# Kernel optimization log

Hardware: AMD Instinct MI355X
Metric: run time of the kernel (lower is better)

The kernel has to match this reference:

```python
import jax, jax.numpy as jnp
import numpy as np

D = 128      # d_hidden
TR = 128     # d_tracker
B = 64       # batch
L = 96       # buffer length (L-1 tokens are shifted; buf[0] is a sentinel)
T = 2 * (L - 1) - 1  # 189 transitions: 95 shifts, 94 reduces


def setup_inputs() -> dict:
    key = jax.random.key(0)
    ks = jax.random.split(key, 9)
    s = 0.1
    buffers = jax.random.normal(ks[0], (L, B, 2 * D), dtype=jnp.float32)
    # valid shift-reduce sequence: S S (R S)^93 R  -> 95 shifts, 94 reduces
    pat = [3, 3] + [2, 3] * (L - 3) + [2]
    assert len(pat) == T
    transitions = jnp.asarray(np.tile(np.array(pat, dtype=np.int32)[:, None], (1, B)))
    # Tracker LSTMCell params (torch gate order i, f, g, o)
    W_ih = jax.random.normal(ks[1], (4 * TR, 3 * D), dtype=jnp.float32) * s
    W_hh = jax.random.normal(ks[2], (4 * TR, TR), dtype=jnp.float32) * s
    b_ih = jax.random.normal(ks[3], (4 * TR,), dtype=jnp.float32) * s
    b_hh = jax.random.normal(ks[4], (4 * TR,), dtype=jnp.float32) * s
    # Composition params (gate order g, i, f1, f2, o)
    Wl = jax.random.normal(ks[5], (5 * D, D), dtype=jnp.float32) * s
    bl = jax.random.normal(ks[6], (5 * D,), dtype=jnp.float32) * s
    Wr = jax.random.normal(ks[7], (5 * D, D), dtype=jnp.float32) * s
    Wt = jax.random.normal(ks[8], (5 * D, TR), dtype=jnp.float32) * s
    return {"buffers": buffers, "transitions": transitions,
            "W_ih": W_ih, "W_hh": W_hh, "b_ih": b_ih, "b_hh": b_hh,
            "Wl": Wl, "bl": bl, "Wr": Wr, "Wt": Wt}


def spinn_forward(buffers, transitions, W_ih, W_hh, b_ih, b_hh, Wl, bl, Wr, Wt):
    Lb, Bb, two_d = buffers.shape
    d = two_d // 2
    tr = W_hh.shape[1]
    bidx = jnp.arange(Bb)

    # fixed-size stack per example; slots 0,1 hold buf[0] padding as in torch
    stack0 = jnp.zeros((Bb, Lb + 2, two_d), dtype=buffers.dtype)
    stack0 = stack0.at[:, 0, :].set(buffers[0]).at[:, 1, :].set(buffers[0])
    sp0 = jnp.full((Bb,), 2, dtype=jnp.int32)        # stack pointer (next free slot)
    bp0 = jnp.full((Bb,), Lb, dtype=jnp.int32)       # buffer size (pop from end)
    th0 = jnp.zeros((Bb, tr), dtype=buffers.dtype)
    tc0 = jnp.zeros((Bb, tr), dtype=buffers.dtype)

    def step(carry, trans):
        stack, sp, bp, th, tc = carry
        buf_top = buffers[bp - 1, bidx]              # [B, 2d] buf[-1]
        s1 = stack[bidx, sp - 1]                     # stack[-1]
        s2 = stack[bidx, sp - 2]                     # stack[-2]
        # tracker LSTMCell on h-parts
        x = jnp.concatenate([buf_top[:, :d], s1[:, :d], s2[:, :d]], axis=1)
        gates = x @ W_ih.T + th @ W_hh.T + (b_ih + b_hh)
        ii, ff, gg, oo = jnp.split(gates, 4, axis=1)
        tc2 = jax.nn.sigmoid(ff) * tc + jax.nn.sigmoid(ii) * jnp.tanh(gg)
        th2 = jax.nn.sigmoid(oo) * jnp.tanh(tc2)
        shift = trans == 3
        red = trans == 2
        # composition (computed for all rows, applied only where red)
        lstm_in = s2[:, :d] @ Wl.T + bl + s1[:, :d] @ Wr.T + th2 @ Wt.T
        g_, i_, f1, f2, o_ = jnp.split(lstm_in, 5, axis=1)
        c = (jax.nn.sigmoid(f1) * s2[:, d:] + jax.nn.sigmoid(f2) * s1[:, d:]
             + jax.nn.sigmoid(i_) * jnp.tanh(g_))
        h = jax.nn.sigmoid(o_) * jnp.tanh(c)
        red_val = jnp.concatenate([h, c], axis=1)
        widx = jnp.where(shift, sp, sp - 2)
        val = jnp.where(shift[:, None], buf_top, red_val)
        mask = shift | red
        cur = stack[bidx, widx]
        stack = stack.at[bidx, widx].set(jnp.where(mask[:, None], val, cur))
        sp = sp + jnp.where(shift, 1, 0).astype(sp.dtype) - jnp.where(red, 1, 0).astype(sp.dtype)
        bp = bp - shift.astype(bp.dtype)
        return (stack, sp, bp, th2, tc2), None

    (stack, sp, bp, th, tc), _ = jax.lax.scan(step, (stack0, sp0, bp0, th0, tc0), transitions)
    return stack[bidx, sp - 1][:, :d]                # h of popped top, [B, d]


def reference(buffers, transitions, W_ih, W_hh, b_ih, b_hh, Wl, bl, Wr, Wt):
    return spinn_forward(buffers, transitions, W_ih, W_hh, b_ih, b_hh, Wl, bl, Wr, Wt)
```

## Files before the change

### kernel.cpp

```cpp
#include <hip/hip_runtime.h>

#define D 128
#define TRK 128
#define NB 64
#define LBUF 96
#define T_STEPS 189
#define NWG 32
#define NTHR 256
#define SLOTS 98

typedef __bf16 bf16x8 __attribute__((ext_vector_type(8)));
typedef float f32x4 __attribute__((ext_vector_type(4)));

__device__ __forceinline__ unsigned short f2bf(float f){
  unsigned x = __builtin_bit_cast(unsigned, f);
  unsigned r = (x + 0x7fffu + ((x >> 16) & 1u)) >> 16;
  return (unsigned short)r;
}
__device__ __forceinline__ float bf2f(unsigned short u){
  unsigned x = ((unsigned)u) << 16;
  return __builtin_bit_cast(float, x);
}
__device__ __forceinline__ float sigf(float x){ return 1.f / (1.f + __expf(-x)); }
__device__ __forceinline__ float tanhfast(float x){ return 1.f - 2.f / (__expf(2.f * x) + 1.f); }

#define WS_BUFH   0u
#define WS_STACKH 1572864u
#define WS_STACKC 3178496u
#define WS_TH     6389760u
#define WS_BAR    6422528u

__device__ __forceinline__ void gbar(unsigned* cnt, unsigned target){
  __syncthreads();
  if (threadIdx.x == 0){
    __hip_atomic_fetch_add(cnt, 1u, __ATOMIC_RELEASE, __HIP_MEMORY_SCOPE_AGENT);
    while (__hip_atomic_load(cnt, __ATOMIC_ACQUIRE, __HIP_MEMORY_SCOPE_AGENT) < target)
      __builtin_amdgcn_s_sleep(1);
  }
  __syncthreads();
}

__global__ __launch_bounds__(NTHR, 1) void spinn_kernel(
    const float* __restrict__ buffers, const int* __restrict__ trans,
    const float* __restrict__ W_ih, const float* __restrict__ W_hh,
    const float* __restrict__ b_ih, const float* __restrict__ b_hh,
    const float* __restrict__ Wl, const float* __restrict__ bl,
    const float* __restrict__ Wr, const float* __restrict__ Wt,
    float* __restrict__ out, unsigned char* __restrict__ ws)
{
  unsigned short* bufh   = (unsigned short*)(ws + WS_BUFH);
  unsigned short* stackh = (unsigned short*)(ws + WS_STACKH);
  float*          stackc = (float*)(ws + WS_STACKC);
  unsigned short* thbuf  = (unsigned short*)(ws + WS_TH);
  unsigned*       barcnt = (unsigned*)(ws + WS_BAR);

  __shared__ alignas(16) unsigned short WA_lds[4 * 4 * 64 * 8];
  __shared__ alignas(16) unsigned short WB_lds[6 * 4 * 64 * 8];
  __shared__ float stage[4][16][32];
  __shared__ float tc_lds[256];
  __shared__ float biasA[16];
  __shared__ float biasB[20];
  __shared__ int tr_lds[64];
  __shared__ int sp_lds[64];
  __shared__ int bp_lds[64];

  const int tid  = threadIdx.x;
  const int blk  = blockIdx.x;
  const int lane = tid & 63;
  const int w    = tid >> 6;
  const int gid  = blk * NTHR + tid;

  for (int idx = tid; idx < 4 * 4 * 64 * 8; idx += NTHR){
    int j = idx & 7, ln = (idx >> 3) & 63, kb = (idx >> 9) & 3, src = idx >> 11;
    int v = ln & 15;
    int col = (v >> 2) * 128 + 4 * blk + (v & 3);
    int k = kb * 32 + (ln >> 4) * 8 + j;
    float val = (src < 3) ? W_ih[col * 384 + src * 128 + k] : W_hh[col * 128 + k];
    WA_lds[idx] = f2bf(val);
  }
  for (int idx = tid; idx < 6 * 4 * 64 * 8; idx += NTHR){
    int j = idx & 7, ln = (idx >> 3) & 63, kb = (idx >> 9) & 3, Tt = (idx >> 11) & 1, src = idx >> 12;
    int v = ln & 15;
    int k = kb * 32 + (ln >> 4) * 8 + j;
    float val = 0.f;
    if (Tt == 0){
      int col = (v >> 2) * 128 + 4 * blk + (v & 3);
      const float* Wm = (src == 0) ? Wl : ((src == 1) ? Wr : Wt);
      val = Wm[col * 128 + k];
    } else if ((v >> 2) == 0){
      int col = 512 + 4 * blk + (v & 3);
      const float* Wm = (src == 0) ? Wl : ((src == 1) ? Wr : Wt);
      val = Wm[col * 128 + k];
    }
    WB_lds[idx] = f2bf(val);
  }
  if (tid < 16){ int col = (tid >> 2) * 128 + 4 * blk + (tid & 3); biasA[tid] = b_ih[col] + b_hh[col]; }
  if (tid < 20){
    int col = (tid < 16) ? ((tid >> 2) * 128 + 4 * blk + (tid & 3)) : (512 + 4 * blk + (tid - 16));
    biasB[tid] = bl[col];
  }
  tc_lds[tid] = 0.f;
  if (tid < 64){ sp_lds[tid] = 2; bp_lds[tid] = LBUF; }

  for (int i = gid; i < LBUF * NB * D; i += NWG * NTHR){
    int k = i & 127; int rb = i >> 7;
    bufh[i] = f2bf(buffers[rb * 256 + k]);
  }
  for (int i = gid; i < NB * D; i += NWG * NTHR){
    int b = i >> 7, k = i & 127;
    unsigned short h = f2bf(buffers[b * 256 + k]);
    float c = buffers[b * 256 + 128 + k];
    stackh[(b * SLOTS + 0) * 128 + k] = h;
    stackh[(b * SLOTS + 1) * 128 + k] = h;
    stackc[(b * SLOTS + 0) * 128 + k] = c;
    stackc[(b * SLOTS + 1) * 128 + k] = c;
  }
  for (int i = gid; i < 2 * NB * TRK; i += NWG * NTHR) thbuf[i] = 0;

  unsigned barn = 0;
  gbar(barcnt, ++barn * NWG);

  const bf16x8* WAf = (const bf16x8*)WA_lds;
  const bf16x8* WBf = (const bf16x8*)WB_lds;
  const int r    = w * 16 + (lane & 15);
  const int koff = (lane >> 4) * 8;
  const int dl   = lane >> 4;
  const int dim  = 4 * blk + dl;

  for (int t = 0; t < T_STEPS; ++t){
    if (tid < 64) tr_lds[tid] = trans[t * 64 + tid];
    __syncthreads();
    const int anyRed = __syncthreads_or((tid < 64) && (tr_lds[tid] == 2));
    const unsigned short* th_rd = thbuf + (t & 1) * NB * TRK;
    unsigned short*       th_wr = thbuf + ((t + 1) & 1) * NB * TRK;

    {
      int sp_r = sp_lds[r], bp_r = bp_lds[r];
      const unsigned short* pb = bufh   + ((bp_r - 1) * 64 + r) * 128 + koff;
      const unsigned short* p1 = stackh + (r * SLOTS + sp_r - 1) * 128 + koff;
      const unsigned short* p2 = stackh + (r * SLOTS + sp_r - 2) * 128 + koff;
      const unsigned short* pt = th_rd  + r * 128 + koff;
      bf16x8 a0[4], a1[4], a2[4], a3[4];
      #pragma unroll
      for (int kb = 0; kb < 4; kb++){
        a0[kb] = *(const bf16x8*)(pb + kb * 32);
        a1[kb] = *(const bf16x8*)(p1 + kb * 32);
        a2[kb] = *(const bf16x8*)(p2 + kb * 32);
        a3[kb] = *(const bf16x8*)(pt + kb * 32);
      }
      f32x4 acc = {0.f, 0.f, 0.f, 0.f};
      #pragma unroll
      for (int kb = 0; kb < 4; kb++) acc = __builtin_amdgcn_mfma_f32_16x16x32_bf16(a0[kb], WAf[(0 * 4 + kb) * 64 + lane], acc, 0, 0, 0);
      #pragma unroll
      for (int kb = 0; kb < 4; kb++) acc = __builtin_amdgcn_mfma_f32_16x16x32_bf16(a1[kb], WAf[(1 * 4 + kb) * 64 + lane], acc, 0, 0, 0);
      #pragma unroll
      for (int kb = 0; kb < 4; kb++) acc = __builtin_amdgcn_mfma_f32_16x16x32_bf16(a2[kb], WAf[(2 * 4 + kb) * 64 + lane], acc, 0, 0, 0);
      #pragma unroll
      for (int kb = 0; kb < 4; kb++) acc = __builtin_amdgcn_mfma_f32_16x16x32_bf16(a3[kb], WAf[(3 * 4 + kb) * 64 + lane], acc, 0, 0, 0);
      #pragma unroll
      for (int j = 0; j < 4; j++) stage[w][(lane >> 4) * 4 + j][lane & 15] = acc[j];
    }
    __syncthreads();
    {
      int r16 = lane & 15;
      float iv = stage[w][r16][0 + dl]  + biasA[0 + dl];
      float fv = stage[w][r16][4 + dl]  + biasA[4 + dl];
      float gv = stage[w][r16][8 + dl]  + biasA[8 + dl];
      float ov = stage[w][r16][12 + dl] + biasA[12 + dl];
      float tco = tc_lds[r * 4 + dl];
      float tc2 = sigf(fv) * tco + sigf(iv) * tanhfast(gv);
      float th2 = sigf(ov) * tanhfast(tc2);
      tc_lds[r * 4 + dl] = tc2;
      th_wr[r * 128 + dim] = f2bf(th2);
      if (tr_lds[r] == 3){
        int slot = sp_lds[r]; int bp_r = bp_lds[r];
        stackh[(r * SLOTS + slot) * 128 + dim] = bufh[((bp_r - 1) * 64 + r) * 128 + dim];
        stackc[(r * SLOTS + slot) * 128 + dim] = buffers[((bp_r - 1) * 64 + r) * 256 + 128 + dim];
      }
    }
    gbar(barcnt, ++barn * NWG);

    if (anyRed){
      {
        int sp_r = sp_lds[r];
        const unsigned short* p2 = stackh + (r * SLOTS + sp_r - 2) * 128 + koff;
        const unsigned short* p1 = stackh + (r * SLOTS + sp_r - 1) * 128 + koff;
        const unsigned short* pt = th_wr + r * 128 + koff;
        bf16x8 a0[4], a1[4], a2[4];
        #pragma unroll
        for (int kb = 0; kb < 4; kb++){
          a0[kb] = *(const bf16x8*)(p2 + kb * 32);
          a1[kb] = *(const bf16x8*)(p1 + kb * 32);
          a2[kb] = *(const bf16x8*)(pt + kb * 32);
        }
        f32x4 acc0 = {0.f, 0.f, 0.f, 0.f}, acc1 = {0.f, 0.f, 0.f, 0.f};
        #pragma unroll
        for (int kb = 0; kb < 4; kb++){
          acc0 = __builtin_amdgcn_mfma_f32_16x16x32_bf16(a0[kb], WBf[(0 * 4 + kb) * 64 + lane], acc0, 0, 0, 0);
          acc1 = __builtin_amdgcn_mfma_f32_16x16x32_bf16(a0[kb], WBf[(1 * 4 + kb) * 64 + lane], acc1, 0, 0, 0);
          acc0 = __builtin_amdgcn_mfma_f32_16x16x32_bf16(a1[kb], WBf[(2 * 4 + kb) * 64 + lane], acc0, 0, 0, 0);
          acc1 = __builtin_amdgcn_mfma_f32_16x16x32_bf16(a1[kb], WBf[(3 * 4 + kb) * 64 + lane], acc1, 0, 0, 0);
          acc0 = __builtin_amdgcn_mfma_f32_16x16x32_bf16(a2[kb], WBf[(4 * 4 + kb) * 64 + lane], acc0, 0, 0, 0);
          acc1 = __builtin_amdgcn_mfma_f32_16x16x32_bf16(a2[kb], WBf[(5 * 4 + kb) * 64 + lane], acc1, 0, 0, 0);
        }
        #pragma unroll
        for (int j = 0; j < 4; j++){
          stage[w][(lane >> 4) * 4 + j][lane & 15]      = acc0[j];
          stage[w][(lane >> 4) * 4 + j][16 + (lane & 15)] = acc1[j];
        }
      }
      __syncthreads();
      {
        int r16 = lane & 15;
        int sp_r = sp_lds[r];
        float gv  = stage[w][r16][0 + dl]  + biasB[0 + dl];
        float iv  = stage[w][r16][4 + dl]  + biasB[4 + dl];
        float f1v = stage[w][r16][8 + dl]  + biasB[8 + dl];
        float f2v = stage[w][r16][12 + dl] + biasB[12 + dl];
        float ov  = stage[w][r16][16 + dl] + biasB[16 + dl];
        float s2c = stackc[(r * SLOTS + sp_r - 2) * 128 + dim];
        float s1c = stackc[(r * SLOTS + sp_r - 1) * 128 + dim];
        float c = sigf(f1v) * s2c + sigf(f2v) * s1c + sigf(iv) * tanhfast(gv);
        float h = sigf(ov) * tanhfast(c);
        if (tr_lds[r] == 2){
          stackh[(r * SLOTS + sp_r - 2) * 128 + dim] = f2bf(h);
          stackc[(r * SLOTS + sp_r - 2) * 128 + dim] = c;
        }
      }
      gbar(barcnt, ++barn * NWG);
    }

    if (tid < 64){
      int tr = tr_lds[tid];
      sp_lds[tid] += (tr == 3) - (tr == 2);
      bp_lds[tid] -= (tr == 3);
    }
    __syncthreads();
  }

  {
    int rr = tid & 63, dle = tid >> 6;
    int dme = 4 * blk + dle;
    out[rr * 128 + dme] = bf2f(stackh[(rr * SLOTS + sp_lds[rr] - 1) * 128 + dme]);
  }
}

extern "C" void kernel_launch(void* const* d_in, const int* in_sizes, int n_in,
                              void* d_out, int out_size, void* d_ws, size_t ws_size,
                              hipStream_t stream){
  const float* buffers = (const float*)d_in[0];
  const int*   trans   = (const int*)d_in[1];
  const float* W_ih    = (const float*)d_in[2];
  const float* W_hh    = (const float*)d_in[3];
  const float* b_ih    = (const float*)d_in[4];
  const float* b_hh    = (const float*)d_in[5];
  const float* Wl      = (const float*)d_in[6];
  const float* bl      = (const float*)d_in[7];
  const float* Wr      = (const float*)d_in[8];
  const float* Wt      = (const float*)d_in[9];
  unsigned char* ws = (unsigned char*)d_ws;
  hipMemsetAsync(ws + WS_BAR, 0, 128, stream);
  spinn_kernel<<<dim3(NWG), dim3(NTHR), 0, stream>>>(
      buffers, trans, W_ih, W_hh, b_ih, b_hh, Wl, bl, Wr, Wt,
      (float*)d_out, ws);
}
```

Baseline: 1.661 ms.

## Partition batch into independent groups with per-group flag barriers and register weights

Restructures the persistent kernel from 32 workgroups of 256 threads into 64 single-wave workgroups arranged as 8 batch groups of 8 rows. Each group of 8 workgroups synchronises only among itself through per-workgroup epoch flags, replacing the grid-wide atomic counter barrier. The composition weights move into registers, shared-memory staging of gate values is removed, and cross-workgroup data is exchanged with L2-coherent loads and stores. The aim is to cut global barrier latency and LDS round trips in the serial 189-step loop, at the cost of heavy register pressure and relaxed-ordering synchronisation that could be fragile.

```diff
diff --git a/kernel.cpp b/kernel.cpp
--- a/kernel.cpp
+++ b/kernel.cpp
@@ -5,12 +5,16 @@
 #define NB 64
 #define LBUF 96
 #define T_STEPS 189
-#define NWG 32
-#define NTHR 256
+#define NWG 64
+#define WPG 8
+#define RPG 8
 #define SLOTS 98
 
 typedef __bf16 bf16x8 __attribute__((ext_vector_type(8)));
 typedef float f32x4 __attribute__((ext_vector_type(4)));
+typedef unsigned u32x4 __attribute__((ext_vector_type(4)));
+typedef unsigned short u16x8 __attribute__((ext_vector_type(8)));
+typedef unsigned short u16x4 __attribute__((ext_vector_type(4)));
 
 __device__ __forceinline__ unsigned short f2bf(float f){
   unsigned x = __builtin_bit_cast(unsigned, f);
@@ -24,23 +28,59 @@
 __device__ __forceinline__ float sigf(float x){ return 1.f / (1.f + __expf(-x)); }
 __device__ __forceinline__ float tanhfast(float x){ return 1.f - 2.f / (__expf(2.f * x) + 1.f); }
 
+__device__ __forceinline__ unsigned ld_l3_u32(const unsigned* p){
+  return __hip_atomic_load(p, __ATOMIC_RELAXED, __HIP_MEMORY_SCOPE_AGENT);
+}
+__device__ __forceinline__ bf16x8 ld_l3_frag(const unsigned short* p){
+  const unsigned* q = (const unsigned*)p;
+  u32x4 w;
+  w[0] = ld_l3_u32(q + 0); w[1] = ld_l3_u32(q + 1);
+  w[2] = ld_l3_u32(q + 2); w[3] = ld_l3_u32(q + 3);
+  return __builtin_bit_cast(bf16x8, w);
+}
+__device__ __forceinline__ void st_l3_b16(unsigned short* p, unsigned short v){
+  unsigned vv = v;
+  asm volatile("global_store_short %0, %1, off sc0 sc1" :: "v"(p), "v"(vv) : "memory");
+}
+
 #define WS_BUFH   0u
 #define WS_STACKH 1572864u
 #define WS_STACKC 3178496u
 #define WS_TH     6389760u
-#define WS_BAR    6422528u
-
-__device__ __forceinline__ void gbar(unsigned* cnt, unsigned target){
-  __syncthreads();
-  if (threadIdx.x == 0){
-    __hip_atomic_fetch_add(cnt, 1u, __ATOMIC_RELEASE, __HIP_MEMORY_SCOPE_AGENT);
-    while (__hip_atomic_load(cnt, __ATOMIC_ACQUIRE, __HIP_MEMORY_SCOPE_AGENT) < target)
-      __builtin_amdgcn_s_sleep(1);
-  }
-  __syncthreads();
-}
-
-__global__ __launch_bounds__(NTHR, 1) void spinn_kernel(
+#define WS_FLAGS  6422528u
+#define WS_FLAGS2 6426624u
+
+__device__ __forceinline__ void gbar(unsigned* fl, int sbase, int m, unsigned ep){
+  asm volatile("s_waitcnt vmcnt(0)" ::: "memory");
+  const int l = threadIdx.x;
+  if (l == 0)
+    __hip_atomic_store(fl + (sbase + m) * 16, ep, __ATOMIC_RELAXED, __HIP_MEMORY_SCOPE_AGENT);
+  for (;;){
+    unsigned v = (l < WPG)
+      ? __hip_atomic_load(fl + (sbase + l) * 16, __ATOMIC_RELAXED, __HIP_MEMORY_SCOPE_AGENT)
+      : ep;
+    if (__all((int)(v >= ep))) break;
+    __builtin_amdgcn_s_sleep(1);
+  }
+  __builtin_amdgcn_sched_barrier(0);
+}
+
+__device__ __forceinline__ void gbar_full(unsigned* fl2){
+  asm volatile("s_waitcnt vmcnt(0)" ::: "memory");
+  __builtin_amdgcn_fence(__ATOMIC_RELEASE, "agent");
+  if (threadIdx.x == 0)
+    __hip_atomic_store(fl2 + blockIdx.x * 16, 1u, __ATOMIC_RELAXED, __HIP_MEMORY_SCOPE_AGENT);
+  const int l = threadIdx.x;
+  for (;;){
+    unsigned v = __hip_atomic_load(fl2 + l * 16, __ATOMIC_RELAXED, __HIP_MEMORY_SCOPE_AGENT);
+    if (__all((int)(v >= 1u))) break;
+    __builtin_amdgcn_s_sleep(1);
+  }
+  __builtin_amdgcn_fence(__ATOMIC_ACQUIRE, "agent");
+  __builtin_amdgcn_sched_barrier(0);
+}
+
+__global__ __launch_bounds__(64, 1) void spinn_kernel(
     const float* __restrict__ buffers, const int* __restrict__ trans,
     const float* __restrict__ W_ih, const float* __restrict__ W_hh,
     const float* __restrict__ b_ih, const float* __restrict__ b_hh,
@@ -48,200 +88,204 @@
     const float* __restrict__ Wr, const float* __restrict__ Wt,
     float* __restrict__ out, unsigned char* __restrict__ ws)
 {
-  unsigned short* bufh   = (unsigned short*)(ws + WS_BUFH);
-  unsigned short* stackh = (unsigned short*)(ws + WS_STACKH);
-  float*          stackc = (float*)(ws + WS_STACKC);
-  unsigned short* thbuf  = (unsigned short*)(ws + WS_TH);
-  unsigned*       barcnt = (unsigned*)(ws + WS_BAR);
-
-  __shared__ alignas(16) unsigned short WA_lds[4 * 4 * 64 * 8];
-  __shared__ alignas(16) unsigned short WB_lds[6 * 4 * 64 * 8];
-  __shared__ float stage[4][16][32];
-  __shared__ float tc_lds[256];
-  __shared__ float biasA[16];
-  __shared__ float biasB[20];
-  __shared__ int tr_lds[64];
-  __shared__ int sp_lds[64];
-  __shared__ int bp_lds[64];
-
-  const int tid  = threadIdx.x;
-  const int blk  = blockIdx.x;
-  const int lane = tid & 63;
-  const int w    = tid >> 6;
-  const int gid  = blk * NTHR + tid;
-
-  for (int idx = tid; idx < 4 * 4 * 64 * 8; idx += NTHR){
-    int j = idx & 7, ln = (idx >> 3) & 63, kb = (idx >> 9) & 3, src = idx >> 11;
-    int v = ln & 15;
-    int col = (v >> 2) * 128 + 4 * blk + (v & 3);
-    int k = kb * 32 + (ln >> 4) * 8 + j;
-    float val = (src < 3) ? W_ih[col * 384 + src * 128 + k] : W_hh[col * 128 + k];
-    WA_lds[idx] = f2bf(val);
-  }
-  for (int idx = tid; idx < 6 * 4 * 64 * 8; idx += NTHR){
-    int j = idx & 7, ln = (idx >> 3) & 63, kb = (idx >> 9) & 3, Tt = (idx >> 11) & 1, src = idx >> 12;
-    int v = ln & 15;
-    int k = kb * 32 + (ln >> 4) * 8 + j;
-    float val = 0.f;
-    if (Tt == 0){
-      int col = (v >> 2) * 128 + 4 * blk + (v & 3);
-      const float* Wm = (src == 0) ? Wl : ((src == 1) ? Wr : Wt);
-      val = Wm[col * 128 + k];
-    } else if ((v >> 2) == 0){
-      int col = 512 + 4 * blk + (v & 3);
-      const float* Wm = (src == 0) ? Wl : ((src == 1) ? Wr : Wt);
-      val = Wm[col * 128 + k];
-    }
-    WB_lds[idx] = f2bf(val);
-  }
-  if (tid < 16){ int col = (tid >> 2) * 128 + 4 * blk + (tid & 3); biasA[tid] = b_ih[col] + b_hh[col]; }
-  if (tid < 20){
-    int col = (tid < 16) ? ((tid >> 2) * 128 + 4 * blk + (tid & 3)) : (512 + 4 * blk + (tid - 16));
-    biasB[tid] = bl[col];
-  }
-  tc_lds[tid] = 0.f;
-  if (tid < 64){ sp_lds[tid] = 2; bp_lds[tid] = LBUF; }
-
-  for (int i = gid; i < LBUF * NB * D; i += NWG * NTHR){
-    int k = i & 127; int rb = i >> 7;
-    bufh[i] = f2bf(buffers[rb * 256 + k]);
-  }
-  for (int i = gid; i < NB * D; i += NWG * NTHR){
-    int b = i >> 7, k = i & 127;
-    unsigned short h = f2bf(buffers[b * 256 + k]);
-    float c = buffers[b * 256 + 128 + k];
-    stackh[(b * SLOTS + 0) * 128 + k] = h;
-    stackh[(b * SLOTS + 1) * 128 + k] = h;
-    stackc[(b * SLOTS + 0) * 128 + k] = c;
-    stackc[(b * SLOTS + 1) * 128 + k] = c;
-  }
-  for (int i = gid; i < 2 * NB * TRK; i += NWG * NTHR) thbuf[i] = 0;
-
-  unsigned barn = 0;
-  gbar(barcnt, ++barn * NWG);
-
-  const bf16x8* WAf = (const bf16x8*)WA_lds;
-  const bf16x8* WBf = (const bf16x8*)WB_lds;
-  const int r    = w * 16 + (lane & 15);
-  const int koff = (lane >> 4) * 8;
-  const int dl   = lane >> 4;
-  const int dim  = 4 * blk + dl;
+  const int l = threadIdx.x;
+  const int g = blockIdx.x & 7;
+  const int m = blockIdx.x >> 3;
+  const int tb = g * RPG;
+
+  unsigned short* bufh_g   = (unsigned short*)(ws + WS_BUFH)   + g * (LBUF * RPG * 128);
+  unsigned short* stackh_g = (unsigned short*)(ws + WS_STACKH) + g * (RPG * SLOTS * 128);
+  float*          stackc_w = (float*)(ws + WS_STACKC)          + (g * 8 + m) * (RPG * SLOTS * 16);
+  unsigned short* th_g     = (unsigned short*)(ws + WS_TH)     + g * (2 * RPG * 128);
+  unsigned*       flags    = (unsigned*)(ws + WS_FLAGS);
+  unsigned*       flags2   = (unsigned*)(ws + WS_FLAGS2);
+
+  __shared__ unsigned short WA_lds[32768];
+
+  const int dd = l & 15;
+  const int rf = l & 7;
+  const int k0 = (l >> 4) * 8;
+
+  for (int c0 = l; c0 < 4096; c0 += 64){
+    int ln = c0 & 63, kb = (c0 >> 6) & 3, s = (c0 >> 8) & 3, q = c0 >> 10;
+    int gr = q * 128 + 16 * m + (ln & 15);
+    int kk = kb * 32 + (ln >> 4) * 8;
+    const float* sp = (s < 3) ? (W_ih + gr * 384 + s * 128 + kk) : (W_hh + gr * 128 + kk);
+    f32x4 f0 = *(const f32x4*)sp, f1 = *(const f32x4*)(sp + 4);
+    u16x8 u;
+    #pragma unroll
+    for (int j = 0; j < 4; ++j){ u[j] = f2bf(f0[j]); u[4 + j] = f2bf(f1[j]); }
+    *(u16x8*)(WA_lds + c0 * 8) = u;
+  }
+
+  bf16x8 wb[5][3][4];
+  #pragma unroll
+  for (int p = 0; p < 5; ++p){
+    int gr = (p < 4 ? p * 128 : 512) + 16 * m + dd;
+    #pragma unroll
+    for (int s = 0; s < 3; ++s){
+      const float* base = (s == 0 ? Wl : (s == 1 ? Wr : Wt)) + gr * 128 + k0;
+      #pragma unroll
+      for (int kb = 0; kb < 4; ++kb){
+        f32x4 f0 = *(const f32x4*)(base + kb * 32);
+        f32x4 f1 = *(const f32x4*)(base + kb * 32 + 4);
+        u16x8 u;
+        #pragma unroll
+        for (int j = 0; j < 4; ++j){ u[j] = f2bf(f0[j]); u[4 + j] = f2bf(f1[j]); }
+        wb[p][s][kb] = __builtin_bit_cast(bf16x8, u);
+      }
+    }
+  }
+
+  float bA[4], bB[5];
+  #pragma unroll
+  for (int q = 0; q < 4; ++q)
+    bA[q] = b_ih[q * 128 + 16 * m + dd] + b_hh[q * 128 + 16 * m + dd];
+  #pragma unroll
+  for (int p = 0; p < 4; ++p) bB[p] = bl[p * 128 + 16 * m + dd];
+  bB[4] = bl[512 + 16 * m + dd];
+
+  for (int i = l * 4; i < 12 * 1024; i += 256){
+    int lrow = m * 12 + (i >> 10);
+    int rr = (i >> 7) & 7;
+    int kk = i & 127;
+    f32x4 f = *(const f32x4*)(buffers + (lrow * 64 + tb + rr) * 256 + kk);
+    u16x4 u;
+    #pragma unroll
+    for (int j = 0; j < 4; ++j) u[j] = f2bf(f[j]);
+    *(u16x4*)(bufh_g + (lrow * 8 + rr) * 128 + kk) = u;
+  }
+
+  for (int i = l; i < 256; i += 64){
+    int slot = i >> 7, rr = (i >> 4) & 7, d2 = i & 15;
+    int ch = 16 * m + d2;
+    stackh_g[(rr * SLOTS + slot) * 128 + ch] = f2bf(buffers[(tb + rr) * 256 + ch]);
+    stackc_w[(rr * SLOTS + slot) * 16 + d2]  = buffers[(tb + rr) * 256 + 128 + ch];
+    th_g[slot * 1024 + rr * 128 + ch] = 0;
+  }
+
+  gbar_full(flags2);
+
+  const bf16x8* WAv = (const bf16x8*)WA_lds;
+
+  int spf = 2, bpf = LBUF;
+  int sp_s[4] = {2, 2, 2, 2}, bp_s[4] = {LBUF, LBUF, LBUF, LBUF};
+  float tcr[4] = {0.f, 0.f, 0.f, 0.f};
+  unsigned ep = 0;
 
   for (int t = 0; t < T_STEPS; ++t){
-    if (tid < 64) tr_lds[tid] = trans[t * 64 + tid];
-    __syncthreads();
-    const int anyRed = __syncthreads_or((tid < 64) && (tr_lds[tid] == 2));
-    const unsigned short* th_rd = thbuf + (t & 1) * NB * TRK;
-    unsigned short*       th_wr = thbuf + ((t + 1) & 1) * NB * TRK;
-
-    {
-      int sp_r = sp_lds[r], bp_r = bp_lds[r];
-      const unsigned short* pb = bufh   + ((bp_r - 1) * 64 + r) * 128 + koff;
-      const unsigned short* p1 = stackh + (r * SLOTS + sp_r - 1) * 128 + koff;
-      const unsigned short* p2 = stackh + (r * SLOTS + sp_r - 2) * 128 + koff;
-      const unsigned short* pt = th_rd  + r * 128 + koff;
-      bf16x8 a0[4], a1[4], a2[4], a3[4];
-      #pragma unroll
-      for (int kb = 0; kb < 4; kb++){
-        a0[kb] = *(const bf16x8*)(pb + kb * 32);
-        a1[kb] = *(const bf16x8*)(p1 + kb * 32);
-        a2[kb] = *(const bf16x8*)(p2 + kb * 32);
-        a3[kb] = *(const bf16x8*)(pt + kb * 32);
-      }
-      f32x4 acc = {0.f, 0.f, 0.f, 0.f};
-      #pragma unroll
-      for (int kb = 0; kb < 4; kb++) acc = __builtin_amdgcn_mfma_f32_16x16x32_bf16(a0[kb], WAf[(0 * 4 + kb) * 64 + lane], acc, 0, 0, 0);
-      #pragma unroll
-      for (int kb = 0; kb < 4; kb++) acc = __builtin_amdgcn_mfma_f32_16x16x32_bf16(a1[kb], WAf[(1 * 4 + kb) * 64 + lane], acc, 0, 0, 0);
-      #pragma unroll
-      for (int kb = 0; kb < 4; kb++) acc = __builtin_amdgcn_mfma_f32_16x16x32_bf16(a2[kb], WAf[(2 * 4 + kb) * 64 + lane], acc, 0, 0, 0);
-      #pragma unroll
-      for (int kb = 0; kb < 4; kb++) acc = __builtin_amdgcn_mfma_f32_16x16x32_bf16(a3[kb], WAf[(3 * 4 + kb) * 64 + lane], acc, 0, 0, 0);
-      #pragma unroll
-      for (int j = 0; j < 4; j++) stage[w][(lane >> 4) * 4 + j][lane & 15] = acc[j];
-    }
-    __syncthreads();
-    {
-      int r16 = lane & 15;
-      float iv = stage[w][r16][0 + dl]  + biasA[0 + dl];
-      float fv = stage[w][r16][4 + dl]  + biasA[4 + dl];
-      float gv = stage[w][r16][8 + dl]  + biasA[8 + dl];
-      float ov = stage[w][r16][12 + dl] + biasA[12 + dl];
-      float tco = tc_lds[r * 4 + dl];
-      float tc2 = sigf(fv) * tco + sigf(iv) * tanhfast(gv);
-      float th2 = sigf(ov) * tanhfast(tc2);
-      tc_lds[r * 4 + dl] = tc2;
-      th_wr[r * 128 + dim] = f2bf(th2);
-      if (tr_lds[r] == 3){
-        int slot = sp_lds[r]; int bp_r = bp_lds[r];
-        stackh[(r * SLOTS + slot) * 128 + dim] = bufh[((bp_r - 1) * 64 + r) * 128 + dim];
-        stackc[(r * SLOTS + slot) * 128 + dim] = buffers[((bp_r - 1) * 64 + r) * 256 + 128 + dim];
-      }
-    }
-    gbar(barcnt, ++barn * NWG);
+    const unsigned short* th_rd = th_g + (t & 1) * 1024;
+    unsigned short*       th_wr = th_g + ((t + 1) & 1) * 1024;
+    int trf = trans[t * 64 + tb + rf];
+    bool anyRed = __any(trf == 2);
+
+    const unsigned short* pb = bufh_g   + ((bpf - 1) * 8 + rf) * 128 + k0;
+    const unsigned short* p1 = stackh_g + (rf * SLOTS + spf - 1) * 128 + k0;
+    const unsigned short* p2 = stackh_g + (rf * SLOTS + spf - 2) * 128 + k0;
+    const unsigned short* pt = th_rd + rf * 128 + k0;
+    bf16x8 ab[4], a1[4], a2[4], at[4];
+    #pragma unroll
+    for (int kb = 0; kb < 4; ++kb){
+      ab[kb] = *(const bf16x8*)(pb + kb * 32);
+      a1[kb] = ld_l3_frag(p1 + kb * 32);
+      a2[kb] = ld_l3_frag(p2 + kb * 32);
+      at[kb] = ld_l3_frag(pt + kb * 32);
+    }
+    f32x4 acc[4];
+    #pragma unroll
+    for (int q = 0; q < 4; ++q){
+      f32x4 a = {0.f, 0.f, 0.f, 0.f};
+      #pragma unroll
+      for (int kb = 0; kb < 4; ++kb) a = __builtin_amdgcn_mfma_f32_16x16x32_bf16(ab[kb], WAv[((q * 4 + 0) * 4 + kb) * 64 + l], a, 0, 0, 0);
+      #pragma unroll
+      for (int kb = 0; kb < 4; ++kb) a = __builtin_amdgcn_mfma_f32_16x16x32_bf16(a1[kb], WAv[((q * 4 + 1) * 4 + kb) * 64 + l], a, 0, 0, 0);
+      #pragma unroll
+      for (int kb = 0; kb < 4; ++kb) a = __builtin_amdgcn_mfma_f32_16x16x32_bf16(a2[kb], WAv[((q * 4 + 2) * 4 + kb) * 64 + l], a, 0, 0, 0);
+      #pragma unroll
+      for (int kb = 0; kb < 4; ++kb) a = __builtin_amdgcn_mfma_f32_16x16x32_bf16(at[kb], WAv[((q * 4 + 3) * 4 + kb) * 64 + l], a, 0, 0, 0);
+      acc[q] = a;
+    }
+    if (l < 32){
+      #pragma unroll
+      for (int j = 0; j < 4; ++j){
+        int rj = (l >> 4) * 4 + j;
+        float iv = acc[0][j] + bA[0];
+        float fv = acc[1][j] + bA[1];
+        float gv = acc[2][j] + bA[2];
+        float ov = acc[3][j] + bA[3];
+        float tc2 = sigf(fv) * tcr[j] + sigf(iv) * tanhfast(gv);
+        tcr[j] = tc2;
+        float th2 = sigf(ov) * tanhfast(tc2);
+        st_l3_b16(th_wr + rj * 128 + 16 * m + dd, f2bf(th2));
+        int trj = trans[t * 64 + tb + rj];
+        if (trj == 3){
+          st_l3_b16(stackh_g + (rj * SLOTS + sp_s[j]) * 128 + 16 * m + dd,
+                    bufh_g[((bp_s[j] - 1) * 8 + rj) * 128 + 16 * m + dd]);
+          stackc_w[(rj * SLOTS + sp_s[j]) * 16 + dd] =
+                    buffers[((bp_s[j] - 1) * 64 + tb + rj) * 256 + 128 + 16 * m + dd];
+        }
+      }
+    }
+    gbar(flags, g * 8, m, ++ep);
 
     if (anyRed){
-      {
-        int sp_r = sp_lds[r];
-        const unsigned short* p2 = stackh + (r * SLOTS + sp_r - 2) * 128 + koff;
-        const unsigned short* p1 = stackh + (r * SLOTS + sp_r - 1) * 128 + koff;
-        const unsigned short* pt = th_wr + r * 128 + koff;
-        bf16x8 a0[4], a1[4], a2[4];
-        #pragma unroll
-        for (int kb = 0; kb < 4; kb++){
-          a0[kb] = *(const bf16x8*)(p2 + kb * 32);
-          a1[kb] = *(const bf16x8*)(p1 + kb * 32);
-          a2[kb] = *(const bf16x8*)(pt + kb * 32);
+      const unsigned short* pt2 = th_wr + rf * 128 + k0;
+      bf16x8 at2[4];
+      #pragma unroll
+      for (int kb = 0; kb < 4; ++kb) at2[kb] = ld_l3_frag(pt2 + kb * 32);
+      f32x4 c5[5];
+      #pragma unroll
+      for (int p = 0; p < 5; ++p){
+        f32x4 a = {0.f, 0.f, 0.f, 0.f};
+        #pragma unroll
+        for (int kb = 0; kb < 4; ++kb) a = __builtin_amdgcn_mfma_f32_16x16x32_bf16(a2[kb],  wb[p][0][kb], a, 0, 0, 0);
+        #pragma unroll
+        for (int kb = 0; kb < 4; ++kb) a = __builtin_amdgcn_mfma_f32_16x16x32_bf16(a1[kb],  wb[p][1][kb], a, 0, 0, 0);
+        #pragma unroll
+        for (int kb = 0; kb < 4; ++kb) a = __builtin_amdgcn_mfma_f32_16x16x32_bf16(at2[kb], wb[p][2][kb], a, 0, 0, 0);
+        c5[p] = a;
+      }
+      if (l < 32){
+        #pragma unroll
+        for (int j = 0; j < 4; ++j){
+          int rj = (l >> 4) * 4 + j;
+          int trj = trans[t * 64 + tb + rj];
+          float gv  = c5[0][j] + bB[0];
+          float iv  = c5[1][j] + bB[1];
+          float f1v = c5[2][j] + bB[2];
+          float f2v = c5[3][j] + bB[3];
+          float ov  = c5[4][j] + bB[4];
+          float s2c = stackc_w[(rj * SLOTS + sp_s[j] - 2) * 16 + dd];
+          float s1c = stackc_w[(rj * SLOTS + sp_s[j] - 1) * 16 + dd];
+          float cc = sigf(f1v) * s2c + sigf(f2v) * s1c + sigf(iv) * tanhfast(gv);
+          float hh = sigf(ov) * tanhfast(cc);
+          if (trj == 2){
+            st_l3_b16(stackh_g + (rj * SLOTS + sp_s[j] - 2) * 128 + 16 * m + dd, f2bf(hh));
+            stackc_w[(rj * SLOTS + sp_s[j] - 2) * 16 + dd] = cc;
+          }
         }
-        f32x4 acc0 = {0.f, 0.f, 0.f, 0.f}, acc1 = {0.f, 0.f, 0.f, 0.f};
-        #pragma unroll
-        for (int kb = 0; kb < 4; kb++){
-          acc0 = __builtin_amdgcn_mfma_f32_16x16x32_bf16(a0[kb], WBf[(0 * 4 + kb) * 64 + lane], acc0, 0, 0, 0);
-          acc1 = __builtin_amdgcn_mfma_f32_16x16x32_bf16(a0[kb], WBf[(1 * 4 + kb) * 64 + lane], acc1, 0, 0, 0);
-          acc0 = __builtin_amdgcn_mfma_f32_16x16x32_bf16(a1[kb], WBf[(2 * 4 + kb) * 64 + lane], acc0, 0, 0, 0);
-          acc1 = __builtin_amdgcn_mfma_f32_16x16x32_bf16(a1[kb], WBf[(3 * 4 + kb) * 64 + lane], acc1, 0, 0, 0);
-          acc0 = __builtin_amdgcn_mfma_f32_16x16x32_bf16(a2[kb], WBf[(4 * 4 + kb) * 64 + lane], acc0, 0, 0, 0);
-          acc1 = __builtin_amdgcn_mfma_f32_16x16x32_bf16(a2[kb], WBf[(5 * 4 + kb) * 64 + lane], acc1, 0, 0, 0);
-        }
-        #pragma unroll
-        for (int j = 0; j < 4; j++){
-          stage[w][(lane >> 4) * 4 + j][lane & 15]      = acc0[j];
-          stage[w][(lane >> 4) * 4 + j][16 + (lane & 15)] = acc1[j];
-        }
-      }
-      __syncthreads();
-      {
-        int r16 = lane & 15;
-        int sp_r = sp_lds[r];
-        float gv  = stage[w][r16][0 + dl]  + biasB[0 + dl];
-        float iv  = stage[w][r16][4 + dl]  + biasB[4 + dl];
-        float f1v = stage[w][r16][8 + dl]  + biasB[8 + dl];
-        float f2v = stage[w][r16][12 + dl] + biasB[12 + dl];
-        float ov  = stage[w][r16][16 + dl] + biasB[16 + dl];
-        float s2c = stackc[(r * SLOTS + sp_r - 2) * 128 + dim];
-        float s1c = stackc[(r * SLOTS + sp_r - 1) * 128 + dim];
-        float c = sigf(f1v) * s2c + sigf(f2v) * s1c + sigf(iv) * tanhfast(gv);
-        float h = sigf(ov) * tanhfast(c);
-        if (tr_lds[r] == 2){
-          stackh[(r * SLOTS + sp_r - 2) * 128 + dim] = f2bf(h);
-          stackc[(r * SLOTS + sp_r - 2) * 128 + dim] = c;
-        }
-      }
-      gbar(barcnt, ++barn * NWG);
-    }
-
-    if (tid < 64){
-      int tr = tr_lds[tid];
-      sp_lds[tid] += (tr == 3) - (tr == 2);
-      bp_lds[tid] -= (tr == 3);
-    }
-    __syncthreads();
+      }
+      gbar(flags, g * 8, m, ++ep);
+    }
+
+    spf += (trf == 3) - (trf == 2);
+    bpf -= (trf == 3);
+    if (l < 32){
+      #pragma unroll
+      for (int j = 0; j < 4; ++j){
+        int trj = trans[t * 64 + tb + (l >> 4) * 4 + j];
+        sp_s[j] += (trj == 3) - (trj == 2);
+        bp_s[j] -= (trj == 3);
+      }
+    }
   }
 
   {
-    int rr = tid & 63, dle = tid >> 6;
-    int dme = 4 * blk + dle;
-    out[rr * 128 + dme] = bf2f(stackh[(rr * SLOTS + sp_lds[rr] - 1) * 128 + dme]);
+    int dd0 = (l >> 3) * 2;
+    const unsigned* p = (const unsigned*)(stackh_g + (rf * SLOTS + spf - 1) * 128 + 16 * m + dd0);
+    unsigned w = ld_l3_u32(p);
+    out[(tb + rf) * 128 + 16 * m + dd0]     = bf2f((unsigned short)(w & 0xffff));
+    out[(tb + rf) * 128 + 16 * m + dd0 + 1] = bf2f((unsigned short)(w >> 16));
   }
 }
 
@@ -259,8 +303,8 @@
   const float* Wr      = (const float*)d_in[8];
   const float* Wt      = (const float*)d_in[9];
   unsigned char* ws = (unsigned char*)d_ws;
-  hipMemsetAsync(ws + WS_BAR, 0, 128, stream);
-  spinn_kernel<<<dim3(NWG), dim3(NTHR), 0, stream>>>(
+  hipMemsetAsync(ws + WS_FLAGS, 0, 8192, stream);
+  spinn_kernel<<<dim3(NWG), dim3(64), 0, stream>>>(
       buffers, trans, W_ih, W_hh, b_ih, b_hh, Wl, bl, Wr, Wt,
       (float*)d_out, ws);
 }
```

New measurement: 1.676 ms. No clear change (+0.9%).
